# Performance work log

Hardware: AMD Instinct MI355X
Metric: run time of the kernel (lower is better)

Reference implementation:

```python
import jax, jax.numpy as jnp
import numpy as np

EPS = 1e-6
DATA_DIM = 2048
LATENT_DIM = 64
ENC = [1024, 1024, 2048]
BATCH = 8192
K_ROUNDS = 24  # fixed proposal rounds for Marsaglia-Tsang rejection (accept prob per round > 0.95)


def _sample_gamma_boosted(key, al, be):
    """Marsaglia-Tsang sampler with alpha-boost, matching the torch al<1 branch.

    Samples Gamma(al+1, 1) via squeeze/rejection, then applies the
    u^(1/al) boost and divides by be, exactly as:
    exp(log(d*v + 1e-6) + log(u + 1e-6)/(al + 1e-6)) / (be + 1e-6)
    """
    d = (al + 1.0) - 1.0 / 3.0              # [B, L]
    c = 1.0 / jnp.sqrt(9.0 * d)             # [B, L]
    k1, k2 = jax.random.split(key)
    eps = jax.random.normal(k1, (K_ROUNDS,) + al.shape, dtype=al.dtype)
    u = jax.random.uniform(k2, (K_ROUNDS,) + al.shape, dtype=al.dtype,
                           minval=1e-7, maxval=1.0)
    v = 1.0 + c[None] * eps                 # [K, B, L]
    v3 = v * v * v
    safe_v3 = jnp.where(v > 0, v3, 1.0)
    # squeeze accept OR full log-accept (standard MT test, as in source index1/index2)
    accept = (v > 0) & ((u < 1.0 - 0.0331 * (eps * eps) * (eps * eps)) |
                        (jnp.log(u) < 0.5 * eps * eps + d[None] * (1.0 - safe_v3 + jnp.log(safe_v3))))
    idx = jnp.argmax(accept, axis=0)        # first accepted round per element
    eps_s = jnp.take_along_axis(eps, idx[None], axis=0)[0]
    u_s = jnp.take_along_axis(u, idx[None], axis=0)[0]
    v_s = (1.0 + c * eps_s) ** 3
    return jnp.exp(jnp.log(d * v_s + EPS) + jnp.log(u_s + EPS) / (al + EPS)) / (be + EPS)


def setup_inputs() -> dict:
    key = jax.random.key(0)
    ks = jax.random.split(key, 20)

    def lin(k, fan_in, fan_out):
        kw, kb = jax.random.split(k)
        w = jax.random.normal(kw, (fan_in, fan_out), dtype=jnp.float32) / np.sqrt(fan_in)
        b = jax.random.normal(kb, (fan_out,), dtype=jnp.float32) * 0.01
        return w, b

    inp = {"x": jax.random.uniform(ks[0], (BATCH, DATA_DIM), dtype=jnp.float32)}
    inp["fc1_w"], inp["fc1_b"] = lin(ks[1], DATA_DIM, ENC[0])
    inp["fc2_w"], inp["fc2_b"] = lin(ks[2], ENC[0], ENC[1])
    inp["fc3_w"], inp["fc3_b"] = lin(ks[3], ENC[1], ENC[2])
    inp["fc41_w"], inp["fc41_b"] = lin(ks[4], ENC[2], LATENT_DIM)
    inp["fc42_w"], inp["fc42_b"] = lin(ks[5], ENC[2], LATENT_DIM)
    inp["fc4_w"], inp["fc4_b"] = lin(ks[6], LATENT_DIM, ENC[2])
    inp["fc5_w"], inp["fc5_b"] = lin(ks[7], ENC[2], ENC[1])
    inp["fc6_w"], inp["fc6_b"] = lin(ks[8], ENC[1], ENC[0])
    inp["fc7_w"], inp["fc7_b"] = lin(ks[9], ENC[0], DATA_DIM * 2)
    return inp


def reference(x, fc1_w, fc1_b, fc2_w, fc2_b, fc3_w, fc3_b,
              fc41_w, fc41_b, fc42_w, fc42_b,
              fc4_w, fc4_b, fc5_w, fc5_b, fc6_w, fc6_b, fc7_w, fc7_b):
    relu, sp = jax.nn.relu, jax.nn.softplus
    # encoder
    h1 = relu(x @ fc1_w + fc1_b)
    h2 = relu(h1 @ fc2_w + fc2_b)
    h3 = relu(h2 @ fc3_w + fc3_b)
    logalpha = EPS + sp(h3 @ fc41_w + fc41_b)   # [B, L], positive
    logbeta = EPS + sp(h3 @ fc42_w + fc42_b)
    # reparameterize via Marsaglia-Tsang gamma rejection sampling
    z = _sample_gamma_boosted(jax.random.key(42), logalpha, logbeta)
    # decoder (torch calls decode(z) twice with identical result; compute once)
    h4 = relu(z @ fc4_w + fc4_b)
    h5 = relu(h4 @ fc5_w + fc5_b)
    h6 = relu(h5 @ fc6_w + fc6_b)
    dec = h6 @ fc7_w + fc7_b                    # [B, 2*DATA_DIM]
    recon_al = EPS + sp(dec[:, :DATA_DIM])
    recon_be = EPS + sp(dec[:, DATA_DIM:])
    return (recon_al, recon_be, logalpha, logbeta, z)
```

## Files before the change

kernel.cpp:

```cpp
#include <hip/hip_runtime.h>
#include <stdint.h>

#define DEVFN static __device__ __forceinline__

typedef __attribute__((ext_vector_type(8))) short short8;
typedef __attribute__((ext_vector_type(4))) float floatx4;
typedef _Float16 half8 __attribute__((ext_vector_type(8)));

DEVFN uint32_t rotl32(uint32_t v, int d) { return (v << d) | (v >> (32 - d)); }

DEVFN void tf2x32(uint32_t k0, uint32_t k1, uint32_t x0, uint32_t x1,
                  uint32_t& o0, uint32_t& o1) {
  uint32_t k2 = k0 ^ k1 ^ 0x1BD11BDAu;
  x0 += k0; x1 += k1;
  x0 += x1; x1 = rotl32(x1, 13); x1 ^= x0;
  x0 += x1; x1 = rotl32(x1, 15); x1 ^= x0;
  x0 += x1; x1 = rotl32(x1, 26); x1 ^= x0;
  x0 += x1; x1 = rotl32(x1, 6);  x1 ^= x0;
  x0 += k1; x1 += k2 + 1u;
  x0 += x1; x1 = rotl32(x1, 17); x1 ^= x0;
  x0 += x1; x1 = rotl32(x1, 29); x1 ^= x0;
  x0 += x1; x1 = rotl32(x1, 16); x1 ^= x0;
  x0 += x1; x1 = rotl32(x1, 24); x1 ^= x0;
  x0 += k2; x1 += k0 + 2u;
  x0 += x1; x1 = rotl32(x1, 13); x1 ^= x0;
  x0 += x1; x1 = rotl32(x1, 15); x1 ^= x0;
  x0 += x1; x1 = rotl32(x1, 26); x1 ^= x0;
  x0 += x1; x1 = rotl32(x1, 6);  x1 ^= x0;
  x0 += k0; x1 += k1 + 3u;
  x0 += x1; x1 = rotl32(x1, 17); x1 ^= x0;
  x0 += x1; x1 = rotl32(x1, 29); x1 ^= x0;
  x0 += x1; x1 = rotl32(x1, 16); x1 ^= x0;
  x0 += x1; x1 = rotl32(x1, 24); x1 ^= x0;
  x0 += k1; x1 += k2 + 4u;
  x0 += x1; x1 = rotl32(x1, 13); x1 ^= x0;
  x0 += x1; x1 = rotl32(x1, 15); x1 ^= x0;
  x0 += x1; x1 = rotl32(x1, 26); x1 ^= x0;
  x0 += x1; x1 = rotl32(x1, 6);  x1 ^= x0;
  x0 += k2; x1 += k0 + 5u;
  o0 = x0; o1 = x1;
}

DEVFN float erfinv_f32(float x) {
#pragma clang fp contract(off)
  float w = -log1pf(-(x * x));
  float p;
  if (w < 5.0f) {
    w = w - 2.5f;
    p = 2.81022636e-08f;
    p = 3.43273939e-07f + p * w;
    p = -3.5233877e-06f + p * w;
    p = -4.39150654e-06f + p * w;
    p = 0.00021858087f + p * w;
    p = -0.00125372503f + p * w;
    p = -0.00417768164f + p * w;
    p = 0.246640727f + p * w;
    p = 1.50140941f + p * w;
  } else {
    w = __fsqrt_rn(w) - 3.0f;
    p = -0.000200214257f;
    p = 0.000100950558f + p * w;
    p = 0.00134934322f + p * w;
    p = -0.00367342844f + p * w;
    p = 0.00573950773f + p * w;
    p = -0.0076224613f + p * w;
    p = 0.00943887047f + p * w;
    p = 1.00167406f + p * w;
    p = 2.83297682f + p * w;
  }
  return p * x;
}

DEVFN float softplus_ref(float v) {
#pragma clang fp contract(off)
  return fmaxf(v, 0.0f) + log1pf(expf(-fabsf(v)));
}

DEVFN ushort f2bf(float f) {
  uint32_t u = __float_as_uint(f);
  uint32_t r = (u + 0x7FFFu + ((u >> 16) & 1u)) >> 16;
  return (ushort)r;
}

DEVFN void split2(float a, ushort& hb, ushort& lb) {
  _Float16 h = (_Float16)a;
  float r = (a - (float)h) * 2048.0f;
  _Float16 l = (_Float16)r;
  hb = __builtin_bit_cast(unsigned short, h);
  lb = __builtin_bit_cast(unsigned short, l);
}

DEVFN void gl2lds16(const void* g, void* l) {
  __builtin_amdgcn_global_load_lds(
      (const __attribute__((address_space(1))) void*)g,
      (__attribute__((address_space(3))) void*)l, 16, 0, 0);
}

__global__ __launch_bounds__(256) void split_f16(
    const float* __restrict__ in, ushort* __restrict__ oh,
    ushort* __restrict__ ol, int n4) {
  int idx = blockIdx.x * 256 + threadIdx.x;
  int stride = gridDim.x * 256;
  for (int i = idx; i < n4; i += stride) {
    float4 a = ((const float4*)in)[i];
    ushort h0, h1, h2, h3, l0, l1, l2, l3;
    split2(a.x, h0, l0); split2(a.y, h1, l1);
    split2(a.z, h2, l2); split2(a.w, h3, l3);
    ushort4 hv; hv.x = h0; hv.y = h1; hv.z = h2; hv.w = h3;
    ushort4 lv; lv.x = l0; lv.y = l1; lv.z = l2; lv.w = l3;
    ((ushort4*)oh)[i] = hv;
    ((ushort4*)ol)[i] = lv;
  }
}

__global__ __launch_bounds__(256) void transpose_split_f16(
    const float* __restrict__ in, ushort* __restrict__ oh,
    ushort* __restrict__ ol, int R, int C) {
  __shared__ float tile[32][33];
  const int c0 = blockIdx.x * 32, r0 = blockIdx.y * 32;
  const int tx = threadIdx.x & 31, ty = threadIdx.x >> 5;
#pragma unroll
  for (int i = ty; i < 32; i += 8)
    tile[i][tx] = in[(size_t)(r0 + i) * C + c0 + tx];
  __syncthreads();
#pragma unroll
  for (int i = ty; i < 32; i += 8) {
    ushort hb, lb;
    split2(tile[tx][i], hb, lb);
    size_t o = (size_t)(c0 + i) * R + r0 + tx;
    oh[o] = hb; ol[o] = lb;
  }
}

template <int ACT>
__global__ __launch_bounds__(256) void gemm_f16x3(
    const ushort* __restrict__ Ah, const ushort* __restrict__ Al,
    const ushort* __restrict__ Bh, const ushort* __restrict__ Bl,
    const float* __restrict__ bias, ushort* __restrict__ Oh,
    ushort* __restrict__ Ol, float* __restrict__ Of, int M, int N, int K) {
  __shared__ ushort AsH[128 * 32];
  __shared__ ushort AsL[128 * 32];
  __shared__ ushort BsH[128 * 32];
  __shared__ ushort BsL[128 * 32];
  const int tid = threadIdx.x;
  const int wave = tid >> 6, lane = tid & 63;
  const int m0 = blockIdx.y * 128, n0 = blockIdx.x * 128;
  const int lrow = lane & 15, lq = lane >> 4;
  const int wm = wave & 1, wn = wave >> 1;
  const int srow = lane >> 2;
  const int scol = (lane & 3) * 8;

  floatx4 acc1[4][4], acc2[4][4];
#pragma unroll
  for (int i = 0; i < 4; i++)
#pragma unroll
    for (int j = 0; j < 4; j++) {
      acc1[i][j] = (floatx4){0.f, 0.f, 0.f, 0.f};
      acc2[i][j] = (floatx4){0.f, 0.f, 0.f, 0.f};
    }

  for (int k0 = 0; k0 < K; k0 += 32) {
#pragma unroll
    for (int h = 0; h < 2; h++) {
      int r0 = wave * 32 + h * 16;
      gl2lds16(Ah + (size_t)(m0 + r0 + srow) * K + k0 + scol, &AsH[r0 * 32]);
      gl2lds16(Al + (size_t)(m0 + r0 + srow) * K + k0 + scol, &AsL[r0 * 32]);
      gl2lds16(Bh + (size_t)(n0 + r0 + srow) * K + k0 + scol, &BsH[r0 * 32]);
      gl2lds16(Bl + (size_t)(n0 + r0 + srow) * K + k0 + scol, &BsL[r0 * 32]);
    }
    __syncthreads();
    half8 ah[4], al[4];
#pragma unroll
    for (int i = 0; i < 4; i++) {
      ah[i] = *(const half8*)&AsH[(wm * 64 + i * 16 + lrow) * 32 + lq * 8];
      al[i] = *(const half8*)&AsL[(wm * 64 + i * 16 + lrow) * 32 + lq * 8];
    }
#pragma unroll
    for (int j = 0; j < 4; j++) {
      half8 bh = *(const half8*)&BsH[(wn * 64 + j * 16 + lrow) * 32 + lq * 8];
      half8 bl = *(const half8*)&BsL[(wn * 64 + j * 16 + lrow) * 32 + lq * 8];
#pragma unroll
      for (int i = 0; i < 4; i++) {
        acc1[i][j] = __builtin_amdgcn_mfma_f32_16x16x32_f16(ah[i], bh,
                                                            acc1[i][j], 0, 0, 0);
        acc2[i][j] = __builtin_amdgcn_mfma_f32_16x16x32_f16(ah[i], bl,
                                                            acc2[i][j], 0, 0, 0);
        acc2[i][j] = __builtin_amdgcn_mfma_f32_16x16x32_f16(al[i], bh,
                                                            acc2[i][j], 0, 0, 0);
      }
    }
    __syncthreads();
  }

  const float INV2048 = 4.8828125e-4f;
#pragma unroll
  for (int i = 0; i < 4; i++) {
#pragma unroll
    for (int j = 0; j < 4; j++) {
      int colg = n0 + wn * 64 + j * 16 + lrow;
      float bb = bias[colg];
#pragma unroll
      for (int r = 0; r < 4; r++) {
        int rowg = m0 + wm * 64 + i * 16 + lq * 4 + r;
        float v = acc1[i][j][r] + acc2[i][j][r] * INV2048 + bb;
        v = fmaxf(v, 0.0f);
        if (ACT == 1) {
          ushort hb, lb;
          split2(v, hb, lb);
          size_t o = (size_t)rowg * N + colg;
          Oh[o] = hb; Ol[o] = lb;
        } else {
          Of[(size_t)rowg * N + colg] = v;
        }
      }
    }
  }
}

__global__ __launch_bounds__(256) void dual_mfma(
    const ushort* __restrict__ Ah, const ushort* __restrict__ Al,
    const ushort* __restrict__ Bh, const ushort* __restrict__ Bl,
    float* __restrict__ P) {
  __shared__ ushort AsH[128 * 32];
  __shared__ ushort AsL[128 * 32];
  __shared__ ushort BsH[128 * 32];
  __shared__ ushort BsL[128 * 32];
  const int K = 2048;
  const int tid = threadIdx.x;
  const int wave = tid >> 6, lane = tid & 63;
  const int m0 = blockIdx.y * 128;
  const int kbase = blockIdx.x * 256;
  const int lrow = lane & 15, lq = lane >> 4;
  const int wm = wave & 1, wn = wave >> 1;
  const int srow = lane >> 2;
  const int scol = (lane & 3) * 8;

  floatx4 acc1[4][4], acc2[4][4];
#pragma unroll
  for (int i = 0; i < 4; i++)
#pragma unroll
    for (int j = 0; j < 4; j++) {
      acc1[i][j] = (floatx4){0.f, 0.f, 0.f, 0.f};
      acc2[i][j] = (floatx4){0.f, 0.f, 0.f, 0.f};
    }

  for (int kk = 0; kk < 256; kk += 32) {
    int k0 = kbase + kk;
#pragma unroll
    for (int h = 0; h < 2; h++) {
      int r0 = wave * 32 + h * 16;
      gl2lds16(Ah + (size_t)(m0 + r0 + srow) * K + k0 + scol, &AsH[r0 * 32]);
      gl2lds16(Al + (size_t)(m0 + r0 + srow) * K + k0 + scol, &AsL[r0 * 32]);
      gl2lds16(Bh + (size_t)(r0 + srow) * K + k0 + scol, &BsH[r0 * 32]);
      gl2lds16(Bl + (size_t)(r0 + srow) * K + k0 + scol, &BsL[r0 * 32]);
    }
    __syncthreads();
    half8 ah[4], al[4];
#pragma unroll
    for (int i = 0; i < 4; i++) {
      ah[i] = *(const half8*)&AsH[(wm * 64 + i * 16 + lrow) * 32 + lq * 8];
      al[i] = *(const half8*)&AsL[(wm * 64 + i * 16 + lrow) * 32 + lq * 8];
    }
#pragma unroll
    for (int j = 0; j < 4; j++) {
      half8 bh = *(const half8*)&BsH[(wn * 64 + j * 16 + lrow) * 32 + lq * 8];
      half8 bl = *(const half8*)&BsL[(wn * 64 + j * 16 + lrow) * 32 + lq * 8];
#pragma unroll
      for (int i = 0; i < 4; i++) {
        acc1[i][j] = __builtin_amdgcn_mfma_f32_16x16x32_f16(ah[i], bh,
                                                            acc1[i][j], 0, 0, 0);
        acc2[i][j] = __builtin_amdgcn_mfma_f32_16x16x32_f16(ah[i], bl,
                                                            acc2[i][j], 0, 0, 0);
        acc2[i][j] = __builtin_amdgcn_mfma_f32_16x16x32_f16(al[i], bh,
                                                            acc2[i][j], 0, 0, 0);
      }
    }
    __syncthreads();
  }

  const float INV2048 = 4.8828125e-4f;
#pragma unroll
  for (int i = 0; i < 4; i++) {
#pragma unroll
    for (int j = 0; j < 4; j++) {
      int colg = wn * 64 + j * 16 + lrow;
#pragma unroll
      for (int r = 0; r < 4; r++) {
        int rowg = m0 + wm * 64 + i * 16 + lq * 4 + r;
        float v = acc1[i][j][r] + acc2[i][j][r] * INV2048;
        P[((size_t)blockIdx.x * 8192 + rowg) * 128 + colg] = v;
      }
    }
  }
}

__global__ __launch_bounds__(256) void dual_reduce(
    const float* __restrict__ P, const float* __restrict__ b41,
    const float* __restrict__ b42, float* __restrict__ la,
    float* __restrict__ lb) {
#pragma clang fp contract(off)
  int idx = blockIdx.x * 256 + threadIdx.x;
  int row = idx >> 5;
  int c4 = (idx & 31) * 4;
  float4 s = {0.f, 0.f, 0.f, 0.f};
#pragma unroll
  for (int k = 0; k < 8; k++) {
    float4 p = *(const float4*)&P[((size_t)k * 8192 + row) * 128 + c4];
    s.x += p.x; s.y += p.y; s.z += p.z; s.w += p.w;
  }
  float o[4];
  const float* bb = (c4 < 64) ? (b41 + c4) : (b42 + c4 - 64);
#pragma unroll
  for (int q = 0; q < 4; q++) {
    float v = (&s.x)[q] + bb[q];
    o[q] = 1e-6f + softplus_ref(v);
  }
  float* dst = (c4 < 64) ? (la + (size_t)row * 64 + c4)
                         : (lb + (size_t)row * 64 + (c4 - 64));
  *(float4*)dst = *(float4*)o;
}

__global__ __launch_bounds__(256) void gamma_sampler(
    const float* __restrict__ la, const float* __restrict__ lb,
    float* __restrict__ z, ushort* __restrict__ zb) {
#pragma clang fp contract(off)
  const uint32_t i = blockIdx.x * 256u + threadIdx.x;
  uint32_t k1a, k1b, k2a, k2b;
  tf2x32(0u, 42u, 0u, 0u, k1a, k1b);
  tf2x32(0u, 42u, 0u, 1u, k2a, k2b);

  const float LO = __uint_as_float(0xBF7FFFFFu);
  const float SQRT2 = __uint_as_float(0x3FB504F3u);
  const float USCALE = 1.0f - 1e-7f;

  const float al = la[i];
  const float be = lb[i];
  const float d = (al + 1.0f) - 0.33333334f;
  const float c = 1.0f / __fsqrt_rn(9.0f * d);

  float es = 0.0f, us = 0.0f;
  bool done = false;
  for (int k = 0; k < 24; k++) {
    if (__all(done)) break;
    if (!done) {
      uint32_t n = (uint32_t)k * 524288u + i;
      uint32_t o0, o1, p0, p1;
      tf2x32(k1a, k1b, 0u, n, o0, o1);
      tf2x32(k2a, k2b, 0u, n, p0, p1);
      uint32_t eb = o0 ^ o1;
      uint32_t ub = p0 ^ p1;
      float f = __uint_as_float((eb >> 9) | 0x3F800000u) - 1.0f;
      float un = f * 2.0f + LO;
      un = fmaxf(LO, un);
      float e = SQRT2 * erfinv_f32(un);
      float g = __uint_as_float((ub >> 9) | 0x3F800000u) - 1.0f;
      float u = g * USCALE + 1e-7f;
      u = fmaxf(1e-7f, u);
      if (k == 0) { es = e; us = u; }
      float v = 1.0f + c * e;
      if (v > 0.0f) {
        float v3 = (v * v) * v;
        float e2 = e * e;
        bool acc = false;
        float sq = 1.0f - (0.0331f * e2) * e2;
        if (u < sq) acc = true;
        else {
          float rhs = (0.5f * e) * e + d * ((1.0f - v3) + logf(v3));
          if (logf(u) < rhs) acc = true;
        }
        if (acc) { es = e; us = u; done = true; }
      }
    }
  }
  float vv = 1.0f + c * es;
  float vs = (vv * vv) * vv;
  float t = logf(d * vs + 1e-6f) + logf(us + 1e-6f) / (al + 1e-6f);
  float zv = expf(t) / (be + 1e-6f);
  z[i] = zv;
  zb[i] = f2bf(zv);
}

__global__ __launch_bounds__(256) void transpose_bf16(
    const float* __restrict__ in, ushort* __restrict__ out, int R, int C) {
  __shared__ float tile[32][33];
  const int c0 = blockIdx.x * 32, r0 = blockIdx.y * 32;
  const int tx = threadIdx.x & 31, ty = threadIdx.x >> 5;
#pragma unroll
  for (int i = ty; i < 32; i += 8)
    tile[i][tx] = in[(size_t)(r0 + i) * C + c0 + tx];
  __syncthreads();
#pragma unroll
  for (int i = ty; i < 32; i += 8)
    out[(size_t)(c0 + i) * R + r0 + tx] = f2bf(tile[tx][i]);
}

template <int ACT>
__global__ __launch_bounds__(256) void gemm_bf16(
    const ushort* __restrict__ A, const ushort* __restrict__ Bt,
    const float* __restrict__ bias, ushort* __restrict__ C0b,
    float* __restrict__ C0f, float* __restrict__ C1f,
    int M, int N, int K, int split) {
  __shared__ ushort As[128 * 32];
  __shared__ ushort Bs[128 * 32];
  const int tid = threadIdx.x;
  const int wave = tid >> 6, lane = tid & 63;
  const int m0 = blockIdx.y * 128, n0 = blockIdx.x * 128;
  const int lrow = lane & 15, lq = lane >> 4;
  const int wm = wave & 1, wn = wave >> 1;
  const int srow = lane >> 2;
  const int scol = (lane & 3) * 8;

  floatx4 acc[4][4];
#pragma unroll
  for (int i = 0; i < 4; i++)
#pragma unroll
    for (int j = 0; j < 4; j++) acc[i][j] = (floatx4){0.f, 0.f, 0.f, 0.f};

  for (int k0 = 0; k0 < K; k0 += 32) {
#pragma unroll
    for (int h = 0; h < 2; h++) {
      int r0 = wave * 32 + h * 16;
      gl2lds16(A + (size_t)(m0 + r0 + srow) * K + k0 + scol, &As[r0 * 32]);
      gl2lds16(Bt + (size_t)(n0 + r0 + srow) * K + k0 + scol, &Bs[r0 * 32]);
    }
    __syncthreads();
    short8 a[4], b[4];
#pragma unroll
    for (int i = 0; i < 4; i++) {
      a[i] = *(const short8*)&As[(wm * 64 + i * 16 + lrow) * 32 + lq * 8];
      b[i] = *(const short8*)&Bs[(wn * 64 + i * 16 + lrow) * 32 + lq * 8];
    }
#pragma unroll
    for (int i = 0; i < 4; i++)
#pragma unroll
      for (int j = 0; j < 4; j++)
        acc[i][j] = __builtin_amdgcn_mfma_f32_16x16x32_bf16(a[i], b[j],
                                                            acc[i][j], 0, 0, 0);
    __syncthreads();
  }

#pragma unroll
  for (int i = 0; i < 4; i++) {
#pragma unroll
    for (int j = 0; j < 4; j++) {
      int colg = n0 + wn * 64 + j * 16 + lrow;
      float bb = bias[colg];
#pragma unroll
      for (int r = 0; r < 4; r++) {
        int rowg = m0 + wm * 64 + i * 16 + lq * 4 + r;
        float v = acc[i][j][r] + bb;
        if (ACT == 0) {
          v = fmaxf(v, 0.0f);
          C0b[(size_t)rowg * N + colg] = f2bf(v);
        } else {
          v = 1e-6f + softplus_ref(v);
          if (colg < split) C0f[(size_t)rowg * split + colg] = v;
          else              C1f[(size_t)rowg * split + (colg - split)] = v;
        }
      }
    }
  }
}

extern "C" void kernel_launch(void* const* d_in, const int* in_sizes, int n_in,
                              void* d_out, int out_size, void* d_ws,
                              size_t ws_size, hipStream_t stream) {
  const float* x   = (const float*)d_in[0];
  const float* w1  = (const float*)d_in[1];  const float* b1  = (const float*)d_in[2];
  const float* w2  = (const float*)d_in[3];  const float* b2  = (const float*)d_in[4];
  const float* w3  = (const float*)d_in[5];  const float* b3  = (const float*)d_in[6];
  const float* w41 = (const float*)d_in[7];  const float* b41 = (const float*)d_in[8];
  const float* w42 = (const float*)d_in[9];  const float* b42 = (const float*)d_in[10];
  const float* w4  = (const float*)d_in[11]; const float* b4  = (const float*)d_in[12];
  const float* w5  = (const float*)d_in[13]; const float* b5  = (const float*)d_in[14];
  const float* w6  = (const float*)d_in[15]; const float* b6  = (const float*)d_in[16];
  const float* w7  = (const float*)d_in[17]; const float* b7  = (const float*)d_in[18];
  float* out = (float*)d_out;
  float* ws  = (float*)d_ws;
  ushort* wsu = (ushort*)d_ws;

  float* recon_a = out;
  float* recon_b = out + 16777216;
  float* la      = out + 33554432;
  float* lb      = out + 34078720;
  float* zz      = out + 34603008;

  ushort* xh   = wsu;
  ushort* xl   = wsu + 16777216;
  ushort* w1Th = wsu + 33554432;
  ushort* w1Tl = wsu + 35651584;
  ushort* w2Th = wsu + 37748736;
  ushort* w2Tl = wsu + 38797312;
  ushort* h1h  = wsu + 39845888;
  ushort* h1l  = wsu + 48234496;
  ushort* w3Th = wsu + 16777216;
  ushort* w3Tl = wsu + 18874368;
  ushort* h2h  = wsu;
  ushort* h2l  = wsu + 8388608;
  ushort* h3h  = wsu + 20971520;
  ushort* h3l  = wsu + 37748736;
  ushort* wcatTh = wsu + 16777216;
  ushort* wcatTl = wsu + 17039360;
  float*  Ppart = ws;
  ushort* w4T = wsu + 54525952;
  ushort* w5T = wsu + 54657024;
  ushort* w6T = wsu + 56754176;
  ushort* w7T = wsu + 57802752;
  ushort* zb  = wsu;
  ushort* h4b = wsu + 20971520;
  ushort* h5b = wsu + 524288;
  ushort* h6b = wsu + 8912896;

  dim3 blk(256);
  split_f16<<<dim3(2048), blk, 0, stream>>>(x, xh, xl, 4194304);
  transpose_split_f16<<<dim3(32, 64), blk, 0, stream>>>(w1, w1Th, w1Tl, 2048, 1024);
  transpose_split_f16<<<dim3(32, 32), blk, 0, stream>>>(w2, w2Th, w2Tl, 1024, 1024);
  gemm_f16x3<1><<<dim3(8, 64), blk, 0, stream>>>(xh, xl, w1Th, w1Tl, b1,
                                                 h1h, h1l, nullptr, 8192, 1024, 2048);
  transpose_split_f16<<<dim3(64, 32), blk, 0, stream>>>(w3, w3Th, w3Tl, 1024, 2048);
  gemm_f16x3<1><<<dim3(8, 64), blk, 0, stream>>>(h1h, h1l, w2Th, w2Tl, b2,
                                                 h2h, h2l, nullptr, 8192, 1024, 1024);
  transpose_bf16<<<dim3(64, 2),   blk, 0, stream>>>(w4, w4T, 64,   2048);
  transpose_bf16<<<dim3(32, 64),  blk, 0, stream>>>(w5, w5T, 2048, 1024);
  transpose_bf16<<<dim3(32, 32),  blk, 0, stream>>>(w6, w6T, 1024, 1024);
  transpose_bf16<<<dim3(128, 32), blk, 0, stream>>>(w7, w7T, 1024, 4096);
  gemm_f16x3<1><<<dim3(16, 64), blk, 0, stream>>>(h2h, h2l, w3Th, w3Tl, b3,
                                                  h3h, h3l, nullptr, 8192, 2048, 1024);
  transpose_split_f16<<<dim3(2, 64), blk, 0, stream>>>(w41, wcatTh, wcatTl, 2048, 64);
  transpose_split_f16<<<dim3(2, 64), blk, 0, stream>>>(w42, wcatTh + 64 * 2048,
                                                       wcatTl + 64 * 2048, 2048, 64);
  dual_mfma<<<dim3(8, 64), blk, 0, stream>>>(h3h, h3l, wcatTh, wcatTl, Ppart);
  dual_reduce<<<dim3(1024), blk, 0, stream>>>(Ppart, b41, b42, la, lb);
  gamma_sampler<<<dim3(2048), blk, 0, stream>>>(la, lb, zz, zb);
  gemm_bf16<0><<<dim3(16, 64), blk, 0, stream>>>(zb,  w4T, b4, h4b, nullptr, nullptr, 8192, 2048, 64, 0);
  gemm_bf16<0><<<dim3(8, 64),  blk, 0, stream>>>(h4b, w5T, b5, h5b, nullptr, nullptr, 8192, 1024, 2048, 0);
  gemm_bf16<0><<<dim3(8, 64),  blk, 0, stream>>>(h5b, w6T, b6, h6b, nullptr, nullptr, 8192, 1024, 1024, 0);
  gemm_bf16<3><<<dim3(32, 64), blk, 0, stream>>>(h6b, w7T, b7, nullptr, recon_a, recon_b, 8192, 4096, 1024, 2048);
  (void)in_sizes; (void)n_in; (void)out_size; (void)ws_size;
}
```

Before: 1.077 ms.

## Swizzle LDS tiles, remap blocks across XCDs, fuse reduce into sampler, fast softplus

XOR-swizzles the LDS column placement in all MFMA GEMM kernels so fragment reads avoid bank conflicts, and remaps workgroup IDs so neighbouring tiles land on the same XCD for better L2 reuse. It folds the dual_reduce pass into gamma_sampler, removing a launch and a round trip of the alpha/beta tensors through memory, and moves zb to a non-overlapping workspace region. It also switches the final decoder softplus to fast exp/log intrinsics, which may slightly change output accuracy.

```diff
diff --git a/kernel.cpp b/kernel.cpp
--- a/kernel.cpp
+++ b/kernel.cpp
@@ -76,6 +76,11 @@
   return fmaxf(v, 0.0f) + log1pf(expf(-fabsf(v)));
 }
 
+DEVFN float softplus_fast(float v) {
+  float e = __expf(-fabsf(v));
+  return fmaxf(v, 0.0f) + __logf(1.0f + e);
+}
+
 DEVFN ushort f2bf(float f) {
   uint32_t u = __float_as_uint(f);
   uint32_t r = (u + 0x7FFFu + ((u >> 16) & 1u)) >> 16;
@@ -95,6 +100,12 @@
       (const __attribute__((address_space(1))) void*)g,
       (__attribute__((address_space(3))) void*)l, 16, 0, 0);
 }
+
+DEVFN int xcd_swizzle(int bid, int nwg) {
+  if ((nwg & 7) == 0) return (bid & 7) * (nwg >> 3) + (bid >> 3);
+  return bid;
+}
+
 
 __global__ __launch_bounds__(256) void split_f16(
     const float* __restrict__ in, ushort* __restrict__ oh,
@@ -144,11 +155,14 @@
   __shared__ ushort BsL[128 * 32];
   const int tid = threadIdx.x;
   const int wave = tid >> 6, lane = tid & 63;
-  const int m0 = blockIdx.y * 128, n0 = blockIdx.x * 128;
+  const int nbx = gridDim.x;
+  const int bid = xcd_swizzle(blockIdx.y * nbx + blockIdx.x, nbx * gridDim.y);
+  const int m0 = (bid / nbx) * 128, n0 = (bid % nbx) * 128;
   const int lrow = lane & 15, lq = lane >> 4;
   const int wm = wave & 1, wn = wave >> 1;
   const int srow = lane >> 2;
-  const int scol = (lane & 3) * 8;
+  const int scol = (((lane & 3) ^ ((lane >> 3) & 3)) << 3);
+  const int lqs8 = ((lq ^ ((lrow >> 1) & 3)) << 3);
 
   floatx4 acc1[4][4], acc2[4][4];
 #pragma unroll
@@ -172,13 +186,13 @@
     half8 ah[4], al[4];
 #pragma unroll
     for (int i = 0; i < 4; i++) {
-      ah[i] = *(const half8*)&AsH[(wm * 64 + i * 16 + lrow) * 32 + lq * 8];
-      al[i] = *(const half8*)&AsL[(wm * 64 + i * 16 + lrow) * 32 + lq * 8];
-    }
-#pragma unroll
-    for (int j = 0; j < 4; j++) {
-      half8 bh = *(const half8*)&BsH[(wn * 64 + j * 16 + lrow) * 32 + lq * 8];
-      half8 bl = *(const half8*)&BsL[(wn * 64 + j * 16 + lrow) * 32 + lq * 8];
+      ah[i] = *(const half8*)&AsH[(wm * 64 + i * 16 + lrow) * 32 + lqs8];
+      al[i] = *(const half8*)&AsL[(wm * 64 + i * 16 + lrow) * 32 + lqs8];
+    }
+#pragma unroll
+    for (int j = 0; j < 4; j++) {
+      half8 bh = *(const half8*)&BsH[(wn * 64 + j * 16 + lrow) * 32 + lqs8];
+      half8 bl = *(const half8*)&BsL[(wn * 64 + j * 16 + lrow) * 32 + lqs8];
 #pragma unroll
       for (int i = 0; i < 4; i++) {
         acc1[i][j] = __builtin_amdgcn_mfma_f32_16x16x32_f16(ah[i], bh,
@@ -233,7 +247,8 @@
   const int lrow = lane & 15, lq = lane >> 4;
   const int wm = wave & 1, wn = wave >> 1;
   const int srow = lane >> 2;
-  const int scol = (lane & 3) * 8;
+  const int scol = (((lane & 3) ^ ((lane >> 3) & 3)) << 3);
+  const int lqs8 = ((lq ^ ((lrow >> 1) & 3)) << 3);
 
   floatx4 acc1[4][4], acc2[4][4];
 #pragma unroll
@@ -258,13 +273,13 @@
     half8 ah[4], al[4];
 #pragma unroll
     for (int i = 0; i < 4; i++) {
-      ah[i] = *(const half8*)&AsH[(wm * 64 + i * 16 + lrow) * 32 + lq * 8];
-      al[i] = *(const half8*)&AsL[(wm * 64 + i * 16 + lrow) * 32 + lq * 8];
-    }
-#pragma unroll
-    for (int j = 0; j < 4; j++) {
-      half8 bh = *(const half8*)&BsH[(wn * 64 + j * 16 + lrow) * 32 + lq * 8];
-      half8 bl = *(const half8*)&BsL[(wn * 64 + j * 16 + lrow) * 32 + lq * 8];
+      ah[i] = *(const half8*)&AsH[(wm * 64 + i * 16 + lrow) * 32 + lqs8];
+      al[i] = *(const half8*)&AsL[(wm * 64 + i * 16 + lrow) * 32 + lqs8];
+    }
+#pragma unroll
+    for (int j = 0; j < 4; j++) {
+      half8 bh = *(const half8*)&BsH[(wn * 64 + j * 16 + lrow) * 32 + lqs8];
+      half8 bl = *(const half8*)&BsL[(wn * 64 + j * 16 + lrow) * 32 + lqs8];
 #pragma unroll
       for (int i = 0; i < 4; i++) {
         acc1[i][j] = __builtin_amdgcn_mfma_f32_16x16x32_f16(ah[i], bh,
@@ -294,37 +309,24 @@
   }
 }
 
-__global__ __launch_bounds__(256) void dual_reduce(
+__global__ __launch_bounds__(256) void gamma_sampler(
     const float* __restrict__ P, const float* __restrict__ b41,
     const float* __restrict__ b42, float* __restrict__ la,
-    float* __restrict__ lb) {
-#pragma clang fp contract(off)
-  int idx = blockIdx.x * 256 + threadIdx.x;
-  int row = idx >> 5;
-  int c4 = (idx & 31) * 4;
-  float4 s = {0.f, 0.f, 0.f, 0.f};
-#pragma unroll
-  for (int k = 0; k < 8; k++) {
-    float4 p = *(const float4*)&P[((size_t)k * 8192 + row) * 128 + c4];
-    s.x += p.x; s.y += p.y; s.z += p.z; s.w += p.w;
-  }
-  float o[4];
-  const float* bb = (c4 < 64) ? (b41 + c4) : (b42 + c4 - 64);
-#pragma unroll
-  for (int q = 0; q < 4; q++) {
-    float v = (&s.x)[q] + bb[q];
-    o[q] = 1e-6f + softplus_ref(v);
-  }
-  float* dst = (c4 < 64) ? (la + (size_t)row * 64 + c4)
-                         : (lb + (size_t)row * 64 + (c4 - 64));
-  *(float4*)dst = *(float4*)o;
-}
-
-__global__ __launch_bounds__(256) void gamma_sampler(
-    const float* __restrict__ la, const float* __restrict__ lb,
-    float* __restrict__ z, ushort* __restrict__ zb) {
+    float* __restrict__ lb, float* __restrict__ z, ushort* __restrict__ zb) {
 #pragma clang fp contract(off)
   const uint32_t i = blockIdx.x * 256u + threadIdx.x;
+  const int row = i >> 6, col = i & 63;
+  float sa = 0.0f, sb = 0.0f;
+#pragma unroll
+  for (int k = 0; k < 8; k++) {
+    sa += P[((size_t)k * 8192 + row) * 128 + col];
+    sb += P[((size_t)k * 8192 + row) * 128 + 64 + col];
+  }
+  const float al = 1e-6f + softplus_ref(sa + b41[col]);
+  const float be = 1e-6f + softplus_ref(sb + b42[col]);
+  la[i] = al;
+  lb[i] = be;
+
   uint32_t k1a, k1b, k2a, k2b;
   tf2x32(0u, 42u, 0u, 0u, k1a, k1b);
   tf2x32(0u, 42u, 0u, 1u, k2a, k2b);
@@ -333,8 +335,6 @@
   const float SQRT2 = __uint_as_float(0x3FB504F3u);
   const float USCALE = 1.0f - 1e-7f;
 
-  const float al = la[i];
-  const float be = lb[i];
   const float d = (al + 1.0f) - 0.33333334f;
   const float c = 1.0f / __fsqrt_rn(9.0f * d);
 
@@ -404,11 +404,14 @@
   __shared__ ushort Bs[128 * 32];
   const int tid = threadIdx.x;
   const int wave = tid >> 6, lane = tid & 63;
-  const int m0 = blockIdx.y * 128, n0 = blockIdx.x * 128;
+  const int nbx = gridDim.x;
+  const int bid = xcd_swizzle(blockIdx.y * nbx + blockIdx.x, nbx * gridDim.y);
+  const int m0 = (bid / nbx) * 128, n0 = (bid % nbx) * 128;
   const int lrow = lane & 15, lq = lane >> 4;
   const int wm = wave & 1, wn = wave >> 1;
   const int srow = lane >> 2;
-  const int scol = (lane & 3) * 8;
+  const int scol = (((lane & 3) ^ ((lane >> 3) & 3)) << 3);
+  const int lqs8 = ((lq ^ ((lrow >> 1) & 3)) << 3);
 
   floatx4 acc[4][4];
 #pragma unroll
@@ -427,8 +430,8 @@
     short8 a[4], b[4];
 #pragma unroll
     for (int i = 0; i < 4; i++) {
-      a[i] = *(const short8*)&As[(wm * 64 + i * 16 + lrow) * 32 + lq * 8];
-      b[i] = *(const short8*)&Bs[(wn * 64 + i * 16 + lrow) * 32 + lq * 8];
+      a[i] = *(const short8*)&As[(wm * 64 + i * 16 + lrow) * 32 + lqs8];
+      b[i] = *(const short8*)&Bs[(wn * 64 + i * 16 + lrow) * 32 + lqs8];
     }
 #pragma unroll
     for (int i = 0; i < 4; i++)
@@ -453,7 +456,7 @@
           v = fmaxf(v, 0.0f);
           C0b[(size_t)rowg * N + colg] = f2bf(v);
         } else {
-          v = 1e-6f + softplus_ref(v);
+          v = 1e-6f + softplus_fast(v);
           if (colg < split) C0f[(size_t)rowg * split + colg] = v;
           else              C1f[(size_t)rowg * split + (colg - split)] = v;
         }
@@ -506,7 +509,7 @@
   ushort* w5T = wsu + 54657024;
   ushort* w6T = wsu + 56754176;
   ushort* w7T = wsu + 57802752;
-  ushort* zb  = wsu;
+  ushort* zb  = wsu + 37748736;
   ushort* h4b = wsu + 20971520;
   ushort* h5b = wsu + 524288;
   ushort* h6b = wsu + 8912896;
@@ -530,8 +533,7 @@
   transpose_split_f16<<<dim3(2, 64), blk, 0, stream>>>(w42, wcatTh + 64 * 2048,
                                                        wcatTl + 64 * 2048, 2048, 64);
   dual_mfma<<<dim3(8, 64), blk, 0, stream>>>(h3h, h3l, wcatTh, wcatTl, Ppart);
-  dual_reduce<<<dim3(1024), blk, 0, stream>>>(Ppart, b41, b42, la, lb);
-  gamma_sampler<<<dim3(2048), blk, 0, stream>>>(la, lb, zz, zb);
+  gamma_sampler<<<dim3(2048), blk, 0, stream>>>(Ppart, b41, b42, la, lb, zz, zb);
   gemm_bf16<0><<<dim3(16, 64), blk, 0, stream>>>(zb,  w4T, b4, h4b, nullptr, nullptr, 8192, 2048, 64, 0);
   gemm_bf16<0><<<dim3(8, 64),  blk, 0, stream>>>(h4b, w5T, b5, h5b, nullptr, nullptr, 8192, 1024, 2048, 0);
   gemm_bf16<0><<<dim3(8, 64),  blk, 0, stream>>>(h5b, w6T, b6, h6b, nullptr, nullptr, 8192, 1024, 1024, 0);
```

Result: faster. 955.3 us (-11.3%).
